# Kernel tuning notes

Hardware: AMD Instinct MI355X
Metric: run time of the kernel (lower is better)

The kernel has to match this reference:

```python
import jax, jax.numpy as jnp
import numpy as np

PAD_IDX = 0
NUM_VISITS, MAX_CODES = 16384, 48
VOCAB, DIM, HID = 20000, 128, 128


def setup_inputs() -> dict:
    key = jax.random.key(0)
    ks = jax.random.split(key, 16)
    ids = jax.random.randint(ks[0], (NUM_VISITS, MAX_CODES), 0, VOCAB)
    # guarantee every visit has at least one non-pad code (original returns
    # zeros for empty visits; we simply avoid that degenerate case)
    ids = ids.at[:, 0].set(jnp.maximum(ids[:, 0], 1))
    s = 0.05
    return {
        "ids": ids,
        "emb": jax.random.normal(ks[1], (VOCAB, DIM), jnp.float32) * s,
        "W1": jax.random.normal(ks[2], (DIM, HID), jnp.float32) * s,
        "b1": jnp.zeros((HID,), jnp.float32),
        "W2": jax.random.normal(ks[3], (HID, HID), jnp.float32) * s,
        "b2": jnp.zeros((HID,), jnp.float32),
        "Wa1": jax.random.normal(ks[4], (HID, HID), jnp.float32) * s,
        "ba1": jnp.zeros((HID,), jnp.float32),
        "wa2": jax.random.normal(ks[5], (HID,), jnp.float32) * s,
        "ba2": jnp.zeros((1,), jnp.float32),
        "Wr1": jax.random.normal(ks[6], (HID, HID), jnp.float32) * s,
        "br1": jnp.zeros((HID,), jnp.float32),
        "Wr2": jax.random.normal(ks[7], (HID, DIM), jnp.float32) * s,
        "br2": jnp.zeros((DIM,), jnp.float32),
    }


def reference(ids, emb, W1, b1, W2, b2, Wa1, ba1, wa2, ba2, Wr1, br1, Wr2, br2):
    # ids: [V, C] padded code indices; pad_idx codes are masked out.
    mask = ids != PAD_IDX                              # [V, C]
    x = emb[ids]                                       # [V, C, D]
    # phi: Linear->SiLU->Linear->SiLU
    h = jax.nn.silu(x @ W1 + b1)
    h = jax.nn.silu(h @ W2 + b2)                       # [V, C, H]
    # attention pooling: Linear->Tanh->Linear(1), masked softmax over codes
    a = jnp.tanh(h @ Wa1 + ba1) @ wa2 + ba2[0]         # [V, C]
    a = jnp.where(mask, a, -jnp.inf)
    a = jax.nn.softmax(a, axis=1)                      # pad rows -> weight 0
    h_pool = jnp.einsum("vc,vch->vh", a, h)            # [V, H]
    # rho: Linear->SiLU->Linear
    v = jax.nn.silu(h_pool @ Wr1 + br1) @ Wr2 + br2    # [V, D]
    return v
```

## Files before the change

kernel.cpp:

```cpp
#include <hip/hip_runtime.h>
#include <math.h>


#define DIM 128
#define MT 16
#define XLDP 136

typedef float f32x4 __attribute__((ext_vector_type(4)));
typedef short short8 __attribute__((ext_vector_type(8)));

#define MFMA(a, b, c) __builtin_amdgcn_mfma_f32_16x16x32_bf16(a, b, c, 0, 0, 0)

__device__ __forceinline__ float fast_rcp(float x) {
  return __builtin_amdgcn_rcpf(x);
}
__device__ __forceinline__ float silu_f(float v) {
  return v * fast_rcp(1.0f + __expf(-v));
}
__device__ __forceinline__ float tanh_f(float v) {
  float t = __expf(2.0f * v);
  return 1.0f - 2.0f * fast_rcp(t + 1.0f);
}

__device__ __forceinline__ unsigned short bf16_hi(float x, float* hif) {
  unsigned u = __builtin_bit_cast(unsigned, x);
  unsigned h = (u + 0x8000u) >> 16;
  *hif = __builtin_bit_cast(float, h << 16);
  return (unsigned short)h;
}
__device__ __forceinline__ unsigned short bf16_rd(float x) {
  unsigned u = __builtin_bit_cast(unsigned, x);
  return (unsigned short)((u + 0x8000u) >> 16);
}
__device__ __forceinline__ unsigned short f2h(float x) {
  return __builtin_bit_cast(unsigned short, (_Float16)x);
}
__device__ __forceinline__ float h2f(unsigned short u) {
  return (float)__builtin_bit_cast(_Float16, u);
}

__global__ __launch_bounds__(256) void prep_wfrags(
    const float* __restrict__ W1, const float* __restrict__ W2,
    const float* __restrict__ Wa1, const float* __restrict__ Wr1,
    const float* __restrict__ Wr2, unsigned short* __restrict__ frags) {
  const int m = blockIdx.x >> 3, chunk = blockIdx.x & 7;
  const float* W = (m == 0) ? W1 : (m == 1) ? W2 : (m == 2) ? Wa1
                  : (m == 3) ? Wr1 : Wr2;
  unsigned short* fh = frags + (size_t)m * 32768;
  unsigned short* fl = fh + 16384;
  const int fid = chunk * 256 + threadIdx.x;
  const int lane = fid & 63, s = (fid >> 6) & 3, t = fid >> 8;
  const int k0 = s * 32 + (lane >> 4) * 8;
  const int n = t * 16 + (lane & 15);
#pragma unroll
  for (int j = 0; j < 8; ++j) {
    float w = W[(size_t)(k0 + j) * DIM + n];
    float hf;
    unsigned short h = bf16_hi(w, &hf);
    fh[fid * 8 + j] = h;
    fl[fid * 8 + j] = bf16_rd(w - hf);
  }
}

__device__ __forceinline__ void stage_bf16(const float* __restrict__ src,
                                           unsigned short (*xh)[XLDP],
                                           unsigned short (*xl)[XLDP],
                                           int tid) {
  const float4* s = (const float4*)src;
#pragma unroll
  for (int tph = 0; tph < 2; ++tph) {
    int idx = tid + tph * 256;
    int r = idx >> 5, c4 = idx & 31;
    float4 v = s[idx];
    float hf;
    ushort4 h, l;
    h.x = bf16_hi(v.x, &hf); l.x = bf16_rd(v.x - hf);
    h.y = bf16_hi(v.y, &hf); l.y = bf16_rd(v.y - hf);
    h.z = bf16_hi(v.z, &hf); l.z = bf16_rd(v.z - hf);
    h.w = bf16_hi(v.w, &hf); l.w = bf16_rd(v.w - hf);
    *(ushort4*)&xh[r][c4 * 4] = h;
    *(ushort4*)&xl[r][c4 * 4] = l;
  }
}

template <int NT>
__device__ __forceinline__ void gemm_frag(const unsigned short (*xh)[XLDP],
                                          const unsigned short (*xl)[XLDP],
                                          const unsigned short* __restrict__ bhp,
                                          const unsigned short* __restrict__ blp,
                                          int tt0, int lane, f32x4 acc[NT]) {
  const int cr = lane & 15, g = lane >> 4;
  short8 ah[4], al[4];
#pragma unroll
  for (int s = 0; s < 4; ++s) {
    ah[s] = *(const short8*)&xh[cr][s * 32 + g * 8];
    al[s] = *(const short8*)&xl[cr][s * 32 + g * 8];
  }
#pragma unroll
  for (int t = 0; t < NT; ++t) {
    short8 bh[4], bl[4];
#pragma unroll
    for (int s = 0; s < 4; ++s) {
      bh[s] = *(const short8*)(bhp +
          ((size_t)((tt0 + t) * 4 + s) * 64 + lane) * 8);
      bl[s] = *(const short8*)(blp +
          ((size_t)((tt0 + t) * 4 + s) * 64 + lane) * 8);
    }
    f32x4 a = {0.f, 0.f, 0.f, 0.f};
#pragma unroll
    for (int s = 0; s < 4; ++s) {
      a = MFMA(ah[s], bh[s], a);
      a = MFMA(ah[s], bl[s], a);
      a = MFMA(al[s], bh[s], a);
    }
    acc[t] = a;
  }
}

__global__ __launch_bounds__(256) void vocab_mfma(
    const float* __restrict__ emb, const unsigned short* __restrict__ frags,
    const float* __restrict__ b1, const float* __restrict__ b2,
    const float* __restrict__ ba1, const float* __restrict__ wa2,
    const float* __restrict__ ba2, unsigned short* __restrict__ H2h,
    float* __restrict__ L) {
  __shared__ unsigned short Xh[2][MT][XLDP], Xl[2][MT][XLDP];
  __shared__ float sP[4][MT];
  const int tid = threadIdx.x, wid = tid >> 6, lane = tid & 63;
  const int cr = lane & 15, g = lane >> 4;
  const int m0 = blockIdx.x * MT;

  stage_bf16(emb + (size_t)m0 * DIM, Xh[0], Xl[0], tid);
  __syncthreads();

  f32x4 acc[2];
  gemm_frag<2>(Xh[0], Xl[0], frags, frags + 16384, wid * 2, lane, acc);
#pragma unroll
  for (int t = 0; t < 2; ++t) {
    const int col = (wid * 2 + t) * 16 + cr;
    const float bv = b1[col];
#pragma unroll
    for (int r = 0; r < 4; ++r) {
      float o = silu_f(acc[t][r] + bv);
      float hf;
      Xh[1][g * 4 + r][col] = bf16_hi(o, &hf);
      Xl[1][g * 4 + r][col] = bf16_rd(o - hf);
    }
  }
  __syncthreads();
  gemm_frag<2>(Xh[1], Xl[1], frags + 32768, frags + 32768 + 16384,
               wid * 2, lane, acc);
#pragma unroll
  for (int t = 0; t < 2; ++t) {
    const int col = (wid * 2 + t) * 16 + cr;
    const float bv = b2[col];
#pragma unroll
    for (int r = 0; r < 4; ++r) {
      float o = silu_f(acc[t][r] + bv);
      float hf;
      const int row = g * 4 + r;
      Xh[0][row][col] = bf16_hi(o, &hf);
      Xl[0][row][col] = bf16_rd(o - hf);
      H2h[(size_t)(m0 + row) * DIM + col] = f2h(o);
    }
  }
  __syncthreads();
  gemm_frag<2>(Xh[0], Xl[0], frags + 65536, frags + 65536 + 16384,
               wid * 2, lane, acc);
  {
    float pl[4] = {0.f, 0.f, 0.f, 0.f};
#pragma unroll
    for (int t = 0; t < 2; ++t) {
      const int col = (wid * 2 + t) * 16 + cr;
      const float bav = ba1[col], wav = wa2[col];
#pragma unroll
      for (int r = 0; r < 4; ++r)
        pl[r] = fmaf(tanh_f(acc[t][r] + bav), wav, pl[r]);
    }
#pragma unroll
    for (int r = 0; r < 4; ++r) {
      float p = pl[r];
      p += __shfl_xor(p, 1, 64);
      p += __shfl_xor(p, 2, 64);
      p += __shfl_xor(p, 4, 64);
      p += __shfl_xor(p, 8, 64);
      if (cr == 0) sP[wid][g * 4 + r] = p;
    }
  }
  __syncthreads();
  if (tid < MT)
    L[m0 + tid] = sP[0][tid] + sP[1][tid] + sP[2][tid] + sP[3][tid] + ba2[0];
}

__global__ __launch_bounds__(256) void pool_rho(
    const int* __restrict__ ids, const float* __restrict__ L,
    const unsigned short* __restrict__ H2h,
    const unsigned short* __restrict__ frags,
    const float* __restrict__ br1, const float* __restrict__ br2,
    float* __restrict__ out) {
  __shared__ unsigned short Xh[2][MT][XLDP], Xl[2][MT][XLDP];
  const int tid = threadIdx.x, wid = tid >> 6, lane = tid & 63;
  const int cr = lane & 15, g = lane >> 4;
  const int half = lane >> 5, li = lane & 31;
  const int m0 = blockIdx.x * MT;

  for (int k = 0; k < 4; ++k) {
    const int vi = wid * 4 + k;
    const int v = m0 + vi;
    int id = 0;
    float lg = -3.4e38f;
    if (lane < 48) {
      id = ids[(size_t)v * 48 + lane];
      if (id != 0) lg = L[id];
    }
    float mx = lg;
#pragma unroll
    for (int m = 32; m; m >>= 1) mx = fmaxf(mx, __shfl_xor(mx, m, 64));
    float e = (lg > -3.0e38f) ? __expf(lg - mx) : 0.f;
    float s = e;
#pragma unroll
    for (int m = 32; m; m >>= 1) s += __shfl_xor(s, m, 64);
    const float a = e / s;

    float4 acc = make_float4(0.f, 0.f, 0.f, 0.f);
#pragma unroll 8
    for (int c = 0; c < 24; ++c) {
      const int cc = 2 * c + half;
      const float ac = __shfl(a, cc, 64);
      const int idc = __shfl(id, cc, 64);
      const ushort4 hv = ((const ushort4*)(H2h + (size_t)idc * DIM))[li];
      acc.x = fmaf(ac, h2f(hv.x), acc.x);
      acc.y = fmaf(ac, h2f(hv.y), acc.y);
      acc.z = fmaf(ac, h2f(hv.z), acc.z);
      acc.w = fmaf(ac, h2f(hv.w), acc.w);
    }
    acc.x += __shfl_xor(acc.x, 32, 64);
    acc.y += __shfl_xor(acc.y, 32, 64);
    acc.z += __shfl_xor(acc.z, 32, 64);
    acc.w += __shfl_xor(acc.w, 32, 64);
    if (half == 0) {
      float hf;
      ushort4 hh, hl;
      hh.x = bf16_hi(acc.x, &hf); hl.x = bf16_rd(acc.x - hf);
      hh.y = bf16_hi(acc.y, &hf); hl.y = bf16_rd(acc.y - hf);
      hh.z = bf16_hi(acc.z, &hf); hl.z = bf16_rd(acc.z - hf);
      hh.w = bf16_hi(acc.w, &hf); hl.w = bf16_rd(acc.w - hf);
      *(ushort4*)&Xh[0][vi][li * 4] = hh;
      *(ushort4*)&Xl[0][vi][li * 4] = hl;
    }
  }
  __syncthreads();

  f32x4 acc2[2];
  gemm_frag<2>(Xh[0], Xl[0], frags + 3 * 32768, frags + 3 * 32768 + 16384,
               wid * 2, lane, acc2);
#pragma unroll
  for (int t = 0; t < 2; ++t) {
    const int col = (wid * 2 + t) * 16 + cr;
    const float bv = br1[col];
#pragma unroll
    for (int r = 0; r < 4; ++r) {
      float o = silu_f(acc2[t][r] + bv);
      float hf;
      Xh[1][g * 4 + r][col] = bf16_hi(o, &hf);
      Xl[1][g * 4 + r][col] = bf16_rd(o - hf);
    }
  }
  __syncthreads();
  gemm_frag<2>(Xh[1], Xl[1], frags + 4 * 32768, frags + 4 * 32768 + 16384,
               wid * 2, lane, acc2);
#pragma unroll
  for (int t = 0; t < 2; ++t) {
    const int col = (wid * 2 + t) * 16 + cr;
    const float bv = br2[col];
#pragma unroll
    for (int r = 0; r < 4; ++r)
      out[(size_t)(m0 + g * 4 + r) * DIM + col] = acc2[t][r] + bv;
  }
}

extern "C" void kernel_launch(void* const* d_in, const int* in_sizes, int n_in,
                              void* d_out, int out_size, void* d_ws,
                              size_t ws_size, hipStream_t stream) {
  const int*   ids = (const int*)  d_in[0];
  const float* emb = (const float*)d_in[1];
  const float* W1  = (const float*)d_in[2];
  const float* b1  = (const float*)d_in[3];
  const float* W2  = (const float*)d_in[4];
  const float* b2  = (const float*)d_in[5];
  const float* Wa1 = (const float*)d_in[6];
  const float* ba1 = (const float*)d_in[7];
  const float* wa2 = (const float*)d_in[8];
  const float* ba2 = (const float*)d_in[9];
  const float* Wr1 = (const float*)d_in[10];
  const float* br1 = (const float*)d_in[11];
  const float* Wr2 = (const float*)d_in[12];
  const float* br2 = (const float*)d_in[13];
  float* out = (float*)d_out;

  const int VOCAB = 20000, V = 16384;

  unsigned short* H2h = (unsigned short*)d_ws;
  float* L = (float*)(H2h + (size_t)VOCAB * DIM);
  unsigned short* frags = (unsigned short*)(L + VOCAB);

  prep_wfrags<<<40, 256, 0, stream>>>(W1, W2, Wa1, Wr1, Wr2, frags);
  vocab_mfma<<<VOCAB / MT, 256, 0, stream>>>(emb, frags, b1, b2, ba1, wa2,
                                             ba2, H2h, L);
  pool_rho<<<V / MT, 256, 0, stream>>>(ids, L, H2h, frags, br1, br2, out);
}
```

Baseline: 124.8 us.

## Make vocab MLP kernel persistent with register-resident weight fragments and prefetch

The vocab-table MLP kernel becomes a persistent kernel of 250 blocks with 512 threads (8 waves, one 16-column tile each). Each wave loads its W1/W2/Wa1 bf16 hi/lo fragments into registers once and reuses them across all row tiles, and the next tile's embedding rows are prefetched into registers while the current tile is processed. The aim is to stop reloading weight fragments for every 16-row tile and to hide the global load latency. The split-bf16 MFMA chain also uses two independent accumulators to shorten the dependency chain. In exchange, register pressure rises sharply, only 250 blocks run, and each tile needs an extra barrier.

Result: slower. 127.4 us (+2.1%).

```diff
diff --git a/kernel.cpp b/kernel.cpp
--- a/kernel.cpp
+++ b/kernel.cpp
@@ -62,25 +62,36 @@
   }
 }
 
-__device__ __forceinline__ void stage_bf16(const float* __restrict__ src,
-                                           unsigned short (*xh)[XLDP],
-                                           unsigned short (*xl)[XLDP],
-                                           int tid) {
-  const float4* s = (const float4*)src;
-#pragma unroll
-  for (int tph = 0; tph < 2; ++tph) {
-    int idx = tid + tph * 256;
-    int r = idx >> 5, c4 = idx & 31;
-    float4 v = s[idx];
-    float hf;
-    ushort4 h, l;
-    h.x = bf16_hi(v.x, &hf); l.x = bf16_rd(v.x - hf);
-    h.y = bf16_hi(v.y, &hf); l.y = bf16_rd(v.y - hf);
-    h.z = bf16_hi(v.z, &hf); l.z = bf16_rd(v.z - hf);
-    h.w = bf16_hi(v.w, &hf); l.w = bf16_rd(v.w - hf);
-    *(ushort4*)&xh[r][c4 * 4] = h;
-    *(ushort4*)&xl[r][c4 * 4] = l;
-  }
+__device__ __forceinline__ void stage_from_reg(float4 v,
+                                               unsigned short (*xh)[XLDP],
+                                               unsigned short (*xl)[XLDP],
+                                               int tid) {
+  int r = tid >> 5, c4 = tid & 31;
+  float hf;
+  ushort4 h, l;
+  h.x = bf16_hi(v.x, &hf); l.x = bf16_rd(v.x - hf);
+  h.y = bf16_hi(v.y, &hf); l.y = bf16_rd(v.y - hf);
+  h.z = bf16_hi(v.z, &hf); l.z = bf16_rd(v.z - hf);
+  h.w = bf16_hi(v.w, &hf); l.w = bf16_rd(v.w - hf);
+  *(ushort4*)&xh[r][c4 * 4] = h;
+  *(ushort4*)&xl[r][c4 * 4] = l;
+}
+
+__device__ __forceinline__ f32x4 gemm_reg(const unsigned short (*xh)[XLDP],
+                                          const unsigned short (*xl)[XLDP],
+                                          const short8 bh[4],
+                                          const short8 bl[4], int lane) {
+  const int cr = lane & 15, g = lane >> 4;
+  f32x4 a0 = {0.f, 0.f, 0.f, 0.f}, a1 = {0.f, 0.f, 0.f, 0.f};
+#pragma unroll
+  for (int s = 0; s < 4; ++s) {
+    short8 ah = *(const short8*)&xh[cr][s * 32 + g * 8];
+    short8 al = *(const short8*)&xl[cr][s * 32 + g * 8];
+    a0 = MFMA(ah, bh[s], a0);
+    a1 = MFMA(ah, bl[s], a1);
+    a1 = MFMA(al, bh[s], a1);
+  }
+  return a0 + a1;
 }
 
 template <int NT>
@@ -106,89 +117,99 @@
       bl[s] = *(const short8*)(blp +
           ((size_t)((tt0 + t) * 4 + s) * 64 + lane) * 8);
     }
-    f32x4 a = {0.f, 0.f, 0.f, 0.f};
+    f32x4 a0 = {0.f, 0.f, 0.f, 0.f}, a1 = {0.f, 0.f, 0.f, 0.f};
 #pragma unroll
     for (int s = 0; s < 4; ++s) {
-      a = MFMA(ah[s], bh[s], a);
-      a = MFMA(ah[s], bl[s], a);
-      a = MFMA(al[s], bh[s], a);
-    }
-    acc[t] = a;
-  }
-}
-
-__global__ __launch_bounds__(256) void vocab_mfma(
+      a0 = MFMA(ah[s], bh[s], a0);
+      a1 = MFMA(ah[s], bl[s], a1);
+      a1 = MFMA(al[s], bh[s], a1);
+    }
+    acc[t] = a0 + a1;
+  }
+}
+
+__global__ __launch_bounds__(512) void vocab_mfma(
     const float* __restrict__ emb, const unsigned short* __restrict__ frags,
     const float* __restrict__ b1, const float* __restrict__ b2,
     const float* __restrict__ ba1, const float* __restrict__ wa2,
     const float* __restrict__ ba2, unsigned short* __restrict__ H2h,
     float* __restrict__ L) {
   __shared__ unsigned short Xh[2][MT][XLDP], Xl[2][MT][XLDP];
-  __shared__ float sP[4][MT];
+  __shared__ float sP[8][MT];
   const int tid = threadIdx.x, wid = tid >> 6, lane = tid & 63;
   const int cr = lane & 15, g = lane >> 4;
-  const int m0 = blockIdx.x * MT;
-
-  stage_bf16(emb + (size_t)m0 * DIM, Xh[0], Xl[0], tid);
-  __syncthreads();
-
-  f32x4 acc[2];
-  gemm_frag<2>(Xh[0], Xl[0], frags, frags + 16384, wid * 2, lane, acc);
-#pragma unroll
-  for (int t = 0; t < 2; ++t) {
-    const int col = (wid * 2 + t) * 16 + cr;
-    const float bv = b1[col];
-#pragma unroll
-    for (int r = 0; r < 4; ++r) {
-      float o = silu_f(acc[t][r] + bv);
-      float hf;
-      Xh[1][g * 4 + r][col] = bf16_hi(o, &hf);
-      Xl[1][g * 4 + r][col] = bf16_rd(o - hf);
-    }
-  }
-  __syncthreads();
-  gemm_frag<2>(Xh[1], Xl[1], frags + 32768, frags + 32768 + 16384,
-               wid * 2, lane, acc);
-#pragma unroll
-  for (int t = 0; t < 2; ++t) {
-    const int col = (wid * 2 + t) * 16 + cr;
-    const float bv = b2[col];
-#pragma unroll
-    for (int r = 0; r < 4; ++r) {
-      float o = silu_f(acc[t][r] + bv);
-      float hf;
-      const int row = g * 4 + r;
-      Xh[0][row][col] = bf16_hi(o, &hf);
-      Xl[0][row][col] = bf16_rd(o - hf);
-      H2h[(size_t)(m0 + row) * DIM + col] = f2h(o);
-    }
-  }
-  __syncthreads();
-  gemm_frag<2>(Xh[0], Xl[0], frags + 65536, frags + 65536 + 16384,
-               wid * 2, lane, acc);
-  {
-    float pl[4] = {0.f, 0.f, 0.f, 0.f};
-#pragma unroll
-    for (int t = 0; t < 2; ++t) {
-      const int col = (wid * 2 + t) * 16 + cr;
-      const float bav = ba1[col], wav = wa2[col];
-#pragma unroll
-      for (int r = 0; r < 4; ++r)
-        pl[r] = fmaf(tanh_f(acc[t][r] + bav), wav, pl[r]);
-    }
-#pragma unroll
-    for (int r = 0; r < 4; ++r) {
-      float p = pl[r];
-      p += __shfl_xor(p, 1, 64);
-      p += __shfl_xor(p, 2, 64);
-      p += __shfl_xor(p, 4, 64);
-      p += __shfl_xor(p, 8, 64);
-      if (cr == 0) sP[wid][g * 4 + r] = p;
-    }
-  }
-  __syncthreads();
-  if (tid < MT)
-    L[m0 + tid] = sP[0][tid] + sP[1][tid] + sP[2][tid] + sP[3][tid] + ba2[0];
+
+  short8 B1h[4], B1l[4], B2h[4], B2l[4], B3h[4], B3l[4];
+#pragma unroll
+  for (int s = 0; s < 4; ++s) {
+    const size_t off = ((size_t)(wid * 4 + s) * 64 + lane) * 8;
+    B1h[s] = *(const short8*)(frags + off);
+    B1l[s] = *(const short8*)(frags + 16384 + off);
+    B2h[s] = *(const short8*)(frags + 32768 + off);
+    B2l[s] = *(const short8*)(frags + 32768 + 16384 + off);
+    B3h[s] = *(const short8*)(frags + 65536 + off);
+    B3l[s] = *(const short8*)(frags + 65536 + 16384 + off);
+  }
+
+  const int col = wid * 16 + cr;
+  const float bv1 = b1[col], bv2 = b2[col];
+  const float bav = ba1[col], wav = wa2[col];
+
+  float4 pref = ((const float4*)(emb + (size_t)blockIdx.x * MT * DIM))[tid];
+
+  for (int mt = blockIdx.x; mt < 1250; mt += 250) {
+    const int m0 = mt * MT;
+    stage_from_reg(pref, Xh[0], Xl[0], tid);
+    const int mtn = mt + 250;
+    if (mtn < 1250)
+      pref = ((const float4*)(emb + (size_t)mtn * MT * DIM))[tid];
+    __syncthreads();
+
+    {
+      f32x4 acc = gemm_reg(Xh[0], Xl[0], B1h, B1l, lane);
+#pragma unroll
+      for (int r = 0; r < 4; ++r) {
+        float o = silu_f(acc[r] + bv1);
+        float hf;
+        Xh[1][g * 4 + r][col] = bf16_hi(o, &hf);
+        Xl[1][g * 4 + r][col] = bf16_rd(o - hf);
+      }
+    }
+    __syncthreads();
+    {
+      f32x4 acc = gemm_reg(Xh[1], Xl[1], B2h, B2l, lane);
+#pragma unroll
+      for (int r = 0; r < 4; ++r) {
+        float o = silu_f(acc[r] + bv2);
+        float hf;
+        const int row = g * 4 + r;
+        Xh[0][row][col] = bf16_hi(o, &hf);
+        Xl[0][row][col] = bf16_rd(o - hf);
+        H2h[(size_t)(m0 + row) * DIM + col] = f2h(o);
+      }
+    }
+    __syncthreads();
+    {
+      f32x4 acc = gemm_reg(Xh[0], Xl[0], B3h, B3l, lane);
+#pragma unroll
+      for (int r = 0; r < 4; ++r) {
+        float p = tanh_f(acc[r] + bav) * wav;
+        p += __shfl_xor(p, 1, 64);
+        p += __shfl_xor(p, 2, 64);
+        p += __shfl_xor(p, 4, 64);
+        p += __shfl_xor(p, 8, 64);
+        if (cr == 0) sP[wid][g * 4 + r] = p;
+      }
+    }
+    __syncthreads();
+    if (tid < MT) {
+      float s = ba2[0];
+#pragma unroll
+      for (int w = 0; w < 8; ++w) s += sP[w][tid];
+      L[m0 + tid] = s;
+    }
+    __syncthreads();
+  }
 }
 
 __global__ __launch_bounds__(256) void pool_rho(
@@ -304,7 +325,7 @@
   unsigned short* frags = (unsigned short*)(L + VOCAB);
 
   prep_wfrags<<<40, 256, 0, stream>>>(W1, W2, Wa1, Wr1, Wr2, frags);
-  vocab_mfma<<<VOCAB / MT, 256, 0, stream>>>(emb, frags, b1, b2, ba1, wa2,
-                                             ba2, H2h, L);
+  vocab_mfma<<<250, 512, 0, stream>>>(emb, frags, b1, b2, ba1, wa2,
+                                      ba2, H2h, L);
   pool_rho<<<V / MT, 256, 0, stream>>>(ids, L, H2h, frags, br1, br2, out);
 }
```

## Widen pool_rho to 512 threads with 16-byte gathers and split MFMA chains

Applied to the files above, without the earlier changes.

pool_rho now runs 8 waves per block, so each wave pools 2 visits instead of 4 and computes one 16-column tile of each rho GEMM. The gather of bf16 H2 rows uses 16-byte loads, with four codes handled at once per wave and a two-step shuffle reduction. In gemm_frag the three MFMA products are split over two independent accumulators to shorten the dependency chain. The aim is more memory-level parallelism in the gather and less MFMA latency, at the cost of more threads per block and eight accumulators per lane.

After: 123.6 us. Within noise of the previous version (-1.0%).

```diff
diff --git a/kernel.cpp b/kernel.cpp
--- a/kernel.cpp
+++ b/kernel.cpp
@@ -8,6 +8,7 @@
 
 typedef float f32x4 __attribute__((ext_vector_type(4)));
 typedef short short8 __attribute__((ext_vector_type(8)));
+typedef unsigned short u16x8 __attribute__((ext_vector_type(8)));
 
 #define MFMA(a, b, c) __builtin_amdgcn_mfma_f32_16x16x32_bf16(a, b, c, 0, 0, 0)
 
@@ -106,14 +107,14 @@
       bl[s] = *(const short8*)(blp +
           ((size_t)((tt0 + t) * 4 + s) * 64 + lane) * 8);
     }
-    f32x4 a = {0.f, 0.f, 0.f, 0.f};
+    f32x4 a0 = {0.f, 0.f, 0.f, 0.f}, a1 = {0.f, 0.f, 0.f, 0.f};
 #pragma unroll
     for (int s = 0; s < 4; ++s) {
-      a = MFMA(ah[s], bh[s], a);
-      a = MFMA(ah[s], bl[s], a);
-      a = MFMA(al[s], bh[s], a);
-    }
-    acc[t] = a;
+      a0 = MFMA(ah[s], bh[s], a0);
+      a1 = MFMA(ah[s], bl[s], a1);
+      a1 = MFMA(al[s], bh[s], a1);
+    }
+    acc[t] = a0 + a1;
   }
 }
 
@@ -191,7 +192,7 @@
     L[m0 + tid] = sP[0][tid] + sP[1][tid] + sP[2][tid] + sP[3][tid] + ba2[0];
 }
 
-__global__ __launch_bounds__(256) void pool_rho(
+__global__ __launch_bounds__(512) void pool_rho(
     const int* __restrict__ ids, const float* __restrict__ L,
     const unsigned short* __restrict__ H2h,
     const unsigned short* __restrict__ frags,
@@ -200,11 +201,12 @@
   __shared__ unsigned short Xh[2][MT][XLDP], Xl[2][MT][XLDP];
   const int tid = threadIdx.x, wid = tid >> 6, lane = tid & 63;
   const int cr = lane & 15, g = lane >> 4;
-  const int half = lane >> 5, li = lane & 31;
+  const int li = lane & 15;
   const int m0 = blockIdx.x * MT;
 
-  for (int k = 0; k < 4; ++k) {
-    const int vi = wid * 4 + k;
+#pragma unroll
+  for (int k = 0; k < 2; ++k) {
+    const int vi = wid * 2 + k;
     const int v = m0 + vi;
     int id = 0;
     float lg = -3.4e38f;
@@ -221,60 +223,59 @@
     for (int m = 32; m; m >>= 1) s += __shfl_xor(s, m, 64);
     const float a = e / s;
 
-    float4 acc = make_float4(0.f, 0.f, 0.f, 0.f);
-#pragma unroll 8
-    for (int c = 0; c < 24; ++c) {
-      const int cc = 2 * c + half;
+    float a8[8] = {0.f, 0.f, 0.f, 0.f, 0.f, 0.f, 0.f, 0.f};
+#pragma unroll 4
+    for (int c = 0; c < 12; ++c) {
+      const int cc = 4 * c + g;
       const float ac = __shfl(a, cc, 64);
       const int idc = __shfl(id, cc, 64);
-      const ushort4 hv = ((const ushort4*)(H2h + (size_t)idc * DIM))[li];
-      acc.x = fmaf(ac, h2f(hv.x), acc.x);
-      acc.y = fmaf(ac, h2f(hv.y), acc.y);
-      acc.z = fmaf(ac, h2f(hv.z), acc.z);
-      acc.w = fmaf(ac, h2f(hv.w), acc.w);
-    }
-    acc.x += __shfl_xor(acc.x, 32, 64);
-    acc.y += __shfl_xor(acc.y, 32, 64);
-    acc.z += __shfl_xor(acc.z, 32, 64);
-    acc.w += __shfl_xor(acc.w, 32, 64);
-    if (half == 0) {
-      float hf;
-      ushort4 hh, hl;
-      hh.x = bf16_hi(acc.x, &hf); hl.x = bf16_rd(acc.x - hf);
-      hh.y = bf16_hi(acc.y, &hf); hl.y = bf16_rd(acc.y - hf);
-      hh.z = bf16_hi(acc.z, &hf); hl.z = bf16_rd(acc.z - hf);
-      hh.w = bf16_hi(acc.w, &hf); hl.w = bf16_rd(acc.w - hf);
-      *(ushort4*)&Xh[0][vi][li * 4] = hh;
-      *(ushort4*)&Xl[0][vi][li * 4] = hl;
-    }
-  }
-  __syncthreads();
-
-  f32x4 acc2[2];
-  gemm_frag<2>(Xh[0], Xl[0], frags + 3 * 32768, frags + 3 * 32768 + 16384,
-               wid * 2, lane, acc2);
-#pragma unroll
-  for (int t = 0; t < 2; ++t) {
-    const int col = (wid * 2 + t) * 16 + cr;
+      const u16x8 hv = *(const u16x8*)(H2h + (size_t)idc * DIM + li * 8);
+#pragma unroll
+      for (int j = 0; j < 8; ++j)
+        a8[j] = fmaf(ac, h2f(hv[j]), a8[j]);
+    }
+#pragma unroll
+    for (int j = 0; j < 8; ++j) {
+      a8[j] += __shfl_xor(a8[j], 16, 64);
+      a8[j] += __shfl_xor(a8[j], 32, 64);
+    }
+    if (lane < 16) {
+      u16x8 hh, hl;
+#pragma unroll
+      for (int j = 0; j < 8; ++j) {
+        float hf;
+        hh[j] = bf16_hi(a8[j], &hf);
+        hl[j] = bf16_rd(a8[j] - hf);
+      }
+      *(u16x8*)&Xh[0][vi][li * 8] = hh;
+      *(u16x8*)&Xl[0][vi][li * 8] = hl;
+    }
+  }
+  __syncthreads();
+
+  f32x4 acc2[1];
+  gemm_frag<1>(Xh[0], Xl[0], frags + 3 * 32768, frags + 3 * 32768 + 16384,
+               wid, lane, acc2);
+  {
+    const int col = wid * 16 + cr;
     const float bv = br1[col];
 #pragma unroll
     for (int r = 0; r < 4; ++r) {
-      float o = silu_f(acc2[t][r] + bv);
+      float o = silu_f(acc2[0][r] + bv);
       float hf;
       Xh[1][g * 4 + r][col] = bf16_hi(o, &hf);
       Xl[1][g * 4 + r][col] = bf16_rd(o - hf);
     }
   }
   __syncthreads();
-  gemm_frag<2>(Xh[1], Xl[1], frags + 4 * 32768, frags + 4 * 32768 + 16384,
-               wid * 2, lane, acc2);
-#pragma unroll
-  for (int t = 0; t < 2; ++t) {
-    const int col = (wid * 2 + t) * 16 + cr;
+  gemm_frag<1>(Xh[1], Xl[1], frags + 4 * 32768, frags + 4 * 32768 + 16384,
+               wid, lane, acc2);
+  {
+    const int col = wid * 16 + cr;
     const float bv = br2[col];
 #pragma unroll
     for (int r = 0; r < 4; ++r)
-      out[(size_t)(m0 + g * 4 + r) * DIM + col] = acc2[t][r] + bv;
+      out[(size_t)(m0 + g * 4 + r) * DIM + col] = acc2[0][r] + bv;
   }
 }
 
@@ -306,5 +307,5 @@
   prep_wfrags<<<40, 256, 0, stream>>>(W1, W2, Wa1, Wr1, Wr2, frags);
   vocab_mfma<<<VOCAB / MT, 256, 0, stream>>>(emb, frags, b1, b2, ba1, wa2,
                                              ba2, H2h, L);
-  pool_rho<<<V / MT, 256, 0, stream>>>(ids, L, H2h, frags, br1, br2, out);
-}
+  pool_rho<<<V / MT, 512, 0, stream>>>(ids, L, H2h, frags, br1, br2, out);
+}
```
